# Optimization experiments

Hardware: AMD Instinct MI355X
Metric: run time of the kernel (lower is better)

Reference implementation:

```python
import jax, jax.numpy as jnp
import numpy as np

W_MODE, W_COMFORT, W_PROGRESS, W_COLLISION, W_DRIVABLE = 1.0, 0.1, 0.5, 1.0, 0.3
COLLISION_RADIUS = 2.0
LANE_MAX_DIST = 3.0
BIG = 1000000.0


def setup_inputs() -> dict:
    key = jax.random.key(0)
    k1, k2, k3, k4 = jax.random.split(key, 4)
    B, M, T = 16, 60, 80
    N_AGENTS, N_LANES, N_PTS = 128, 64, 20
    return {
        "mode_logits": jax.random.normal(k1, (B, M), dtype=jnp.float32),
        "all_trajs": jax.random.normal(k2, (B, M, T, 3), dtype=jnp.float32),
        "agents_now": jax.random.normal(k3, (B, N_AGENTS, 4), dtype=jnp.float32),
        "agents_mask": jnp.ones((B, N_AGENTS), dtype=jnp.float32),
        "map_lanes": jax.random.normal(k4, (B, N_LANES, N_PTS, 3), dtype=jnp.float32),
        "map_lanes_mask": jnp.ones((B, N_LANES), dtype=jnp.float32),
    }


def reference(mode_logits, all_trajs, agents_now, agents_mask, map_lanes, map_lanes_mask):
    B, M, T, _ = all_trajs.shape
    mode_scores = jax.nn.softmax(mode_logits, axis=-1)  # (B, M)

    ego_xy = all_trajs[..., :2]  # (B, M, T, 2)

    # Comfort: mean jerk norm (3rd finite difference of position)
    vel = ego_xy[:, :, 1:] - ego_xy[:, :, :-1]
    acc = vel[:, :, 1:] - vel[:, :, :-1]
    jerk = acc[:, :, 1:] - acc[:, :, :-1]
    comfort = -jnp.linalg.norm(jerk, axis=-1).mean(axis=-1)  # (B, M)

    # Progress: final x-coordinate
    progress = all_trajs[:, :, -1, 0]  # (B, M)

    # Collision: fraction of timesteps within radius of any valid agent
    agent_xy = agents_now[:, :, :2]  # (B, N, 2)
    # (B, M, T, N): pairwise distance ego trajectory points vs agents
    d_ag = jnp.linalg.norm(ego_xy[:, :, :, None, :] - agent_xy[:, None, None, :, :], axis=-1)
    d_ag = d_ag + (1.0 - agents_mask[:, None, None, :]) * BIG
    min_dist = d_ag.min(axis=-1)  # (B, M, T)
    collision = -(min_dist < COLLISION_RADIUS).astype(jnp.float32).mean(axis=-1)  # (B, M)

    # Drivable: fraction of timesteps farther than lane_max_dist from any valid lane point
    B_, L, P, _ = map_lanes.shape
    lane_flat = map_lanes[..., :2].reshape(B, L * P, 2)  # (B, L*P, 2)
    lane_valid_flat = jnp.repeat(map_lanes_mask, P, axis=1)  # (B, L*P)
    d_ln = jnp.linalg.norm(ego_xy[:, :, :, None, :] - lane_flat[:, None, None, :, :], axis=-1)
    d_ln = d_ln + (1.0 - lane_valid_flat[:, None, None, :]) * BIG
    min_lane_dist = d_ln.min(axis=-1)  # (B, M, T)
    drivable = -(min_lane_dist > LANE_MAX_DIST).astype(jnp.float32).mean(axis=-1)  # (B, M)

    score = (W_MODE * mode_scores + W_COMFORT * comfort + W_PROGRESS * progress
             + W_COLLISION * collision + W_DRIVABLE * drivable)  # (B, M)
    selected_idx = jnp.argmax(score, axis=1)  # (B,)
    selected_traj = all_trajs[jnp.arange(B), selected_idx]  # (B, T, 3)
    return selected_traj, selected_idx
```

## Files before the change

### kernel.cpp

```cpp
#include <hip/hip_runtime.h>
#include <math.h>

#define BM 60
#define TT 80
#define NAG 128
#define NLANES 64
#define NPTS 20
#define NLP (NLANES * NPTS)
#define PPL (NLP / 64)
#define APL (NAG / 64)

__global__ __launch_bounds__(256) void score_kernel(
    const float* __restrict__ trajs,
    const float* __restrict__ agents,
    const float* __restrict__ amask,
    const float* __restrict__ lanes,
    const float* __restrict__ lmask,
    float* __restrict__ scores)
{
    __shared__ float s_ex[TT], s_ey[TT];
    __shared__ float s_j[2];
    __shared__ float s_cc[4], s_cd[4];

    const int bm   = blockIdx.x;
    const int b    = bm / BM;
    const int tid  = threadIdx.x;
    const int w    = tid >> 6;
    const int lane = tid & 63;

    const float* tr = trajs + (size_t)bm * TT * 3;
    for (int i = tid; i < TT; i += 256) {
        s_ex[i] = tr[i * 3 + 0];
        s_ey[i] = tr[i * 3 + 1];
    }

    float ax[APL], ay[APL], aq[APL];
#pragma unroll
    for (int k = 0; k < APL; ++k) {
        const int i = lane + 64 * k;
        const float off = (1.0f - amask[b * NAG + i]) * 1e8f;
        const float x = agents[((size_t)b * NAG + i) * 4 + 0] + off;
        const float y = agents[((size_t)b * NAG + i) * 4 + 1];
        ax[k] = x; ay[k] = y; aq[k] = fmaf(x, x, y * y);
    }
    float px[PPL], py[PPL], pq[PPL];
#pragma unroll
    for (int k = 0; k < PPL; ++k) {
        const int i = lane + 64 * k;
        const float off = (1.0f - lmask[b * NLANES + i / NPTS]) * 1e8f;
        const float x = lanes[((size_t)b * NLP + i) * 3 + 0] + off;
        const float y = lanes[((size_t)b * NLP + i) * 3 + 1];
        px[k] = x; py[k] = y; pq[k] = fmaf(x, x, y * y);
    }

    __syncthreads();

    float jsum = 0.0f;
    if (tid < TT - 3) {
        const float jx = s_ex[tid + 3] - 3.0f * s_ex[tid + 2] + 3.0f * s_ex[tid + 1] - s_ex[tid];
        const float jy = s_ey[tid + 3] - 3.0f * s_ey[tid + 2] + 3.0f * s_ey[tid + 1] - s_ey[tid];
        jsum = sqrtf(jx * jx + jy * jy);
    }
    for (int off = 32; off > 0; off >>= 1) jsum += __shfl_xor(jsum, off, 64);
    if (w < 2 && lane == 0) s_j[w] = jsum;

    int ccoll = 0, cdriv = 0;
    const int t0 = w * (TT / 4);
    for (int r = 0; r < 4; ++r) {
        const int tb = t0 + r * 5;
        float mx5[5], my5[5], thrA[5], thrB[5], m2[5], m3[5];
#pragma unroll
        for (int j = 0; j < 5; ++j) {
            const float ex = s_ex[tb + j];
            const float ey = s_ey[tb + j];
            const float c  = fmaf(ex, ex, ey * ey);
            mx5[j]  = -2.0f * ex;
            my5[j]  = -2.0f * ey;
            thrA[j] = 4.0f - c;
            thrB[j] = 9.0f - c;
            m2[j] = 1e30f;
            m3[j] = 1e30f;
        }
#pragma unroll
        for (int k = 0; k < APL; ++k) {
#pragma unroll
            for (int j = 0; j < 5; ++j) {
                float v = fmaf(my5[j], ay[k], aq[k]);
                v = fmaf(mx5[j], ax[k], v);
                m2[j] = fminf(m2[j], v);
            }
        }
#pragma unroll
        for (int k = 0; k < PPL; ++k) {
#pragma unroll
            for (int j = 0; j < 5; ++j) {
                float v = fmaf(my5[j], py[k], pq[k]);
                v = fmaf(mx5[j], px[k], v);
                m3[j] = fminf(m3[j], v);
            }
        }
#pragma unroll
        for (int j = 0; j < 5; ++j) {
            ccoll += (__ballot(m2[j] < thrA[j]) != 0ull) ? 1 : 0;
            cdriv += (__ballot(m3[j] <= thrB[j]) == 0ull) ? 1 : 0;
        }
    }
    if (lane == 0) { s_cc[w] = (float)ccoll; s_cd[w] = (float)cdriv; }
    __syncthreads();

    if (tid == 0) {
        const float coll = s_cc[0] + s_cc[1] + s_cc[2] + s_cc[3];
        const float driv = s_cd[0] + s_cd[1] + s_cd[2] + s_cd[3];
        const float comfort  = -((s_j[0] + s_j[1]) / (float)(TT - 3));
        const float progress = tr[(TT - 1) * 3 + 0];
        scores[bm] = 0.1f * comfort + 0.5f * progress
                   - 1.0f * (coll / (float)TT)
                   - 0.3f * (driv / (float)TT);
    }
}

__global__ __launch_bounds__(64) void select_kernel(
    const float* __restrict__ logits,
    const float* __restrict__ trajs,
    const float* __restrict__ scores,
    float* __restrict__ out,
    int B)
{
    const int b    = blockIdx.x;
    const int lane = threadIdx.x;

    float lg = (lane < BM) ? logits[b * BM + lane] : -1e30f;
    float mx = lg;
    for (int off = 32; off > 0; off >>= 1) mx = fmaxf(mx, __shfl_xor(mx, off, 64));
    float e = (lane < BM) ? expf(lg - mx) : 0.0f;
    float sum = e;
    for (int off = 32; off > 0; off >>= 1) sum += __shfl_xor(sum, off, 64);

    float sc = (lane < BM) ? (e / sum + scores[b * BM + lane]) : -1e30f;
    int idx = lane;
    for (int off = 32; off > 0; off >>= 1) {
        float os = __shfl_xor(sc, off, 64);
        int   oi = __shfl_xor(idx, off, 64);
        if (os > sc || (os == sc && oi < idx)) { sc = os; idx = oi; }
    }
    const float* src = trajs + ((size_t)b * BM + idx) * TT * 3;
    for (int k = lane; k < TT * 3; k += 64) out[b * TT * 3 + k] = src[k];
    if (lane == 0) out[B * TT * 3 + b] = (float)idx;
}

extern "C" void kernel_launch(void* const* d_in, const int* in_sizes, int n_in,
                              void* d_out, int out_size, void* d_ws, size_t ws_size,
                              hipStream_t stream) {
    const float* logits = (const float*)d_in[0];
    const float* trajs  = (const float*)d_in[1];
    const float* agents = (const float*)d_in[2];
    const float* amask  = (const float*)d_in[3];
    const float* lanes  = (const float*)d_in[4];
    const float* lmask  = (const float*)d_in[5];

    const int B = in_sizes[0] / BM;
    float* scores = (float*)d_ws;
    float* out    = (float*)d_out;

    score_kernel<<<B * BM, 256, 0, stream>>>(trajs, agents, amask, lanes, lmask, scores);
    select_kernel<<<B, 64, 0, stream>>>(logits, trajs, scores, out, B);
}
```

Baseline: 78.27 us.

## Fuse scoring and selection via last-block atomic counter, stage lanes in LDS

Merges the select kernel into the score kernel: each block atomically increments a per-batch counter, and the last block for a batch does the softmax, argmax and trajectory copy. Lane points are loaded with vectorized float4 reads into shared memory instead of being held in registers per thread, and each wave now processes 10 timesteps per pass instead of 5, which raises reuse of each loaded point. The aim is to save a kernel launch and the register pressure of per-thread lane arrays. In exchange it adds a memset, atomics and threadfences, plus shared-memory reads inside the inner loop.

After: 91.81 us. +17.3%, slower.

```diff
diff --git a/kernel.cpp b/kernel.cpp
--- a/kernel.cpp
+++ b/kernel.cpp
@@ -7,20 +7,29 @@
 #define NLANES 64
 #define NPTS 20
 #define NLP (NLANES * NPTS)
-#define PPL (NLP / 64)
 #define APL (NAG / 64)
-
-__global__ __launch_bounds__(256) void score_kernel(
+#define J 10
+#define BIGOFF 1e8f
+
+__global__ __launch_bounds__(256) void fused_kernel(
+    const float* __restrict__ logits,
     const float* __restrict__ trajs,
     const float* __restrict__ agents,
     const float* __restrict__ amask,
     const float* __restrict__ lanes,
     const float* __restrict__ lmask,
-    float* __restrict__ scores)
+    int*   __restrict__ counters,
+    float* __restrict__ scores,
+    float* __restrict__ out,
+    int B)
 {
+    __shared__ float s_px[NLP], s_py[NLP], s_pq[NLP];
     __shared__ float s_ex[TT], s_ey[TT];
+    __shared__ float s_lm[NLANES];
     __shared__ float s_j[2];
     __shared__ float s_cc[4], s_cd[4];
+    __shared__ int   s_sel;
+    __shared__ int   s_idx;
 
     const int bm   = blockIdx.x;
     const int b    = bm / BM;
@@ -28,32 +37,50 @@
     const int w    = tid >> 6;
     const int lane = tid & 63;
 
-    const float* tr = trajs + (size_t)bm * TT * 3;
-    for (int i = tid; i < TT; i += 256) {
-        s_ex[i] = tr[i * 3 + 0];
-        s_ey[i] = tr[i * 3 + 1];
-    }
+    const float4* gl4 = (const float4*)(lanes + (size_t)b * NLP * 3);
+    for (int g = tid; g < (NLP * 3) / 4; g += 256) {
+        const float4 v = gl4[g];
+        const float vv[4] = {v.x, v.y, v.z, v.w};
+#pragma unroll
+        for (int c = 0; c < 4; ++c) {
+            const int f = 4 * g + c;
+            const int p = f / 3;
+            const int r = f - 3 * p;
+            if (r == 0)      s_px[p] = vv[c];
+            else if (r == 1) s_py[p] = vv[c];
+        }
+    }
+    if (tid < (TT * 3) / 4) {
+        const float4 v = ((const float4*)(trajs + (size_t)bm * TT * 3))[tid];
+        const float vv[4] = {v.x, v.y, v.z, v.w};
+#pragma unroll
+        for (int c = 0; c < 4; ++c) {
+            const int f = 4 * tid + c;
+            const int t = f / 3;
+            const int r = f - 3 * t;
+            if (r == 0)      s_ex[t] = vv[c];
+            else if (r == 1) s_ey[t] = vv[c];
+        }
+    }
+    if (tid < NLANES) s_lm[tid] = lmask[b * NLANES + tid];
 
     float ax[APL], ay[APL], aq[APL];
+    const float4* ga4 = (const float4*)(agents + (size_t)b * NAG * 4);
 #pragma unroll
     for (int k = 0; k < APL; ++k) {
-        const int i = lane + 64 * k;
-        const float off = (1.0f - amask[b * NAG + i]) * 1e8f;
-        const float x = agents[((size_t)b * NAG + i) * 4 + 0] + off;
-        const float y = agents[((size_t)b * NAG + i) * 4 + 1];
-        ax[k] = x; ay[k] = y; aq[k] = fmaf(x, x, y * y);
-    }
-    float px[PPL], py[PPL], pq[PPL];
-#pragma unroll
-    for (int k = 0; k < PPL; ++k) {
-        const int i = lane + 64 * k;
-        const float off = (1.0f - lmask[b * NLANES + i / NPTS]) * 1e8f;
-        const float x = lanes[((size_t)b * NLP + i) * 3 + 0] + off;
-        const float y = lanes[((size_t)b * NLP + i) * 3 + 1];
-        px[k] = x; py[k] = y; pq[k] = fmaf(x, x, y * y);
-    }
-
-    __syncthreads();
+        const int i = k * 64 + lane;
+        const float4 a = ga4[i];
+        const float mo = (1.0f - amask[b * NAG + i]) * BIGOFF;
+        ax[k] = a.x; ay[k] = a.y;
+        aq[k] = fmaf(a.x, a.x, a.y * a.y) + mo;
+    }
+    __syncthreads();
+
+    for (int p = tid; p < NLP; p += 256) {
+        const float x = s_px[p], y = s_py[p];
+        const float mo = (1.0f - s_lm[p / NPTS]) * BIGOFF;
+        s_pq[p] = fmaf(x, x, y * y) + mo;
+    }
 
     float jsum = 0.0f;
     if (tid < TT - 3) {
@@ -63,46 +90,47 @@
     }
     for (int off = 32; off > 0; off >>= 1) jsum += __shfl_xor(jsum, off, 64);
     if (w < 2 && lane == 0) s_j[w] = jsum;
+    __syncthreads();
 
     int ccoll = 0, cdriv = 0;
     const int t0 = w * (TT / 4);
-    for (int r = 0; r < 4; ++r) {
-        const int tb = t0 + r * 5;
-        float mx5[5], my5[5], thrA[5], thrB[5], m2[5], m3[5];
-#pragma unroll
-        for (int j = 0; j < 5; ++j) {
+    for (int rr = 0; rr < 2; ++rr) {
+        const int tb = t0 + rr * J;
+        float mx[J], my[J], mA[J], mB[J];
+#pragma unroll
+        for (int j = 0; j < J; ++j) {
             const float ex = s_ex[tb + j];
             const float ey = s_ey[tb + j];
-            const float c  = fmaf(ex, ex, ey * ey);
-            mx5[j]  = -2.0f * ex;
-            my5[j]  = -2.0f * ey;
-            thrA[j] = 4.0f - c;
-            thrB[j] = 9.0f - c;
-            m2[j] = 1e30f;
-            m3[j] = 1e30f;
+            mx[j] = -2.0f * ex;
+            my[j] = -2.0f * ey;
+            mA[j] = 1e30f;
+            mB[j] = 1e30f;
         }
 #pragma unroll
         for (int k = 0; k < APL; ++k) {
 #pragma unroll
-            for (int j = 0; j < 5; ++j) {
-                float v = fmaf(my5[j], ay[k], aq[k]);
-                v = fmaf(mx5[j], ax[k], v);
-                m2[j] = fminf(m2[j], v);
+            for (int j = 0; j < J; ++j) {
+                float v = fmaf(my[j], ay[k], aq[k]);
+                v = fmaf(mx[j], ax[k], v);
+                mA[j] = fminf(mA[j], v);
             }
         }
-#pragma unroll
-        for (int k = 0; k < PPL; ++k) {
-#pragma unroll
-            for (int j = 0; j < 5; ++j) {
-                float v = fmaf(my5[j], py[k], pq[k]);
-                v = fmaf(mx5[j], px[k], v);
-                m3[j] = fminf(m3[j], v);
+        for (int k = 0; k < NLP / 64; ++k) {
+            const int p = k * 64 + lane;
+            const float x = s_px[p], y = s_py[p], q = s_pq[p];
+#pragma unroll
+            for (int j = 0; j < J; ++j) {
+                float v = fmaf(my[j], y, q);
+                v = fmaf(mx[j], x, v);
+                mB[j] = fminf(mB[j], v);
             }
         }
 #pragma unroll
-        for (int j = 0; j < 5; ++j) {
-            ccoll += (__ballot(m2[j] < thrA[j]) != 0ull) ? 1 : 0;
-            cdriv += (__ballot(m3[j] <= thrB[j]) == 0ull) ? 1 : 0;
+        for (int j = 0; j < J; ++j) {
+            const float ex = s_ex[tb + j], ey = s_ey[tb + j];
+            const float c = fmaf(ex, ex, ey * ey);
+            ccoll += (__ballot(mA[j] < 4.0f - c) != 0ull) ? 1 : 0;
+            cdriv += (__ballot(mB[j] <= 9.0f - c) == 0ull) ? 1 : 0;
         }
     }
     if (lane == 0) { s_cc[w] = (float)ccoll; s_cd[w] = (float)cdriv; }
@@ -112,40 +140,43 @@
         const float coll = s_cc[0] + s_cc[1] + s_cc[2] + s_cc[3];
         const float driv = s_cd[0] + s_cd[1] + s_cd[2] + s_cd[3];
         const float comfort  = -((s_j[0] + s_j[1]) / (float)(TT - 3));
-        const float progress = tr[(TT - 1) * 3 + 0];
+        const float progress = s_ex[TT - 1];
         scores[bm] = 0.1f * comfort + 0.5f * progress
                    - 1.0f * (coll / (float)TT)
                    - 0.3f * (driv / (float)TT);
-    }
-}
-
-__global__ __launch_bounds__(64) void select_kernel(
-    const float* __restrict__ logits,
-    const float* __restrict__ trajs,
-    const float* __restrict__ scores,
-    float* __restrict__ out,
-    int B)
-{
-    const int b    = blockIdx.x;
-    const int lane = threadIdx.x;
-
-    float lg = (lane < BM) ? logits[b * BM + lane] : -1e30f;
-    float mx = lg;
-    for (int off = 32; off > 0; off >>= 1) mx = fmaxf(mx, __shfl_xor(mx, off, 64));
-    float e = (lane < BM) ? expf(lg - mx) : 0.0f;
-    float sum = e;
-    for (int off = 32; off > 0; off >>= 1) sum += __shfl_xor(sum, off, 64);
-
-    float sc = (lane < BM) ? (e / sum + scores[b * BM + lane]) : -1e30f;
-    int idx = lane;
-    for (int off = 32; off > 0; off >>= 1) {
-        float os = __shfl_xor(sc, off, 64);
-        int   oi = __shfl_xor(idx, off, 64);
-        if (os > sc || (os == sc && oi < idx)) { sc = os; idx = oi; }
-    }
-    const float* src = trajs + ((size_t)b * BM + idx) * TT * 3;
-    for (int k = lane; k < TT * 3; k += 64) out[b * TT * 3 + k] = src[k];
-    if (lane == 0) out[B * TT * 3 + b] = (float)idx;
+        __threadfence();
+        const int old = atomicAdd(&counters[b], 1);
+        s_sel = (old == BM - 1) ? 1 : 0;
+    }
+    __syncthreads();
+    if (!s_sel) return;
+
+    __threadfence();
+    if (w == 0) {
+        volatile const float* vsc = scores;
+        float lg = (lane < BM) ? logits[b * BM + lane] : -1e30f;
+        float mxv = lg;
+        for (int off = 32; off > 0; off >>= 1) mxv = fmaxf(mxv, __shfl_xor(mxv, off, 64));
+        float e = (lane < BM) ? expf(lg - mxv) : 0.0f;
+        float sum = e;
+        for (int off = 32; off > 0; off >>= 1) sum += __shfl_xor(sum, off, 64);
+        float sc = (lane < BM) ? (e / sum + vsc[b * BM + lane]) : -1e30f;
+        int idx = lane;
+        for (int off = 32; off > 0; off >>= 1) {
+            const float os = __shfl_xor(sc, off, 64);
+            const int   oi = __shfl_xor(idx, off, 64);
+            if (os > sc || (os == sc && oi < idx)) { sc = os; idx = oi; }
+        }
+        if (lane == 0) {
+            s_idx = idx;
+            out[B * TT * 3 + b] = (float)idx;
+        }
+    }
+    __syncthreads();
+    {
+        const float* src = trajs + ((size_t)b * BM + s_idx) * TT * 3;
+        if (tid < TT * 3) out[b * TT * 3 + tid] = src[tid];
+    }
 }
 
 extern "C" void kernel_launch(void* const* d_in, const int* in_sizes, int n_in,
@@ -159,9 +190,11 @@
     const float* lmask  = (const float*)d_in[5];
 
     const int B = in_sizes[0] / BM;
-    float* scores = (float*)d_ws;
-    float* out    = (float*)d_out;
-
-    score_kernel<<<B * BM, 256, 0, stream>>>(trajs, agents, amask, lanes, lmask, scores);
-    select_kernel<<<B, 64, 0, stream>>>(logits, trajs, scores, out, B);
+    int*   counters = (int*)d_ws;
+    float* scores   = (float*)((char*)d_ws + 256);
+    float* out      = (float*)d_out;
+
+    hipMemsetAsync(d_ws, 0, 256, stream);
+    fused_kernel<<<B * BM, 256, 0, stream>>>(logits, trajs, agents, amask,
+                                             lanes, lmask, counters, scores, out, B);
 }
```
